# Kernel tuning notes

Hardware: AMD Instinct MI355X
Metric: run time of the kernel (lower is better)

Reference implementation:

```python
import jax, jax.numpy as jnp
import numpy as np

N, E, IN, ED, HID, HEADS, OUT, G = 50000, 800000, 128, 16, 32, 4, 64, 64
NEG_SLOPE = 0.2


def gat_conv(x, src, dst, edge_attr, W, att_src, att_dst, We, att_edge, bias,
             heads, out_ch, concat):
    """PyG-style GATConv with edge attributes and mean-filled self loops.
    src/dst already include self loops; edge_attr already includes fill rows."""
    n = x.shape[0]
    h = (x @ W).reshape(n, heads, out_ch)                      # [N,H,C]
    a_src = jnp.einsum('nhc,hc->nh', h, att_src)               # [N,H]
    a_dst = jnp.einsum('nhc,hc->nh', h, att_dst)
    eh = (edge_attr @ We).reshape(-1, heads, out_ch)           # [E',H,C]
    a_edge = jnp.einsum('ehc,hc->eh', eh, att_edge)            # [E',H]
    alpha = jax.nn.leaky_relu(a_src[src] + a_dst[dst] + a_edge, NEG_SLOPE)
    # segment softmax over incoming edges of each target node
    amax = jax.ops.segment_max(alpha, dst, num_segments=n)
    ex = jnp.exp(alpha - amax[dst])
    denom = jax.ops.segment_sum(ex, dst, num_segments=n)
    coef = ex / (denom[dst] + 1e-16)                           # [E',H]
    msg = h[src] * coef[:, :, None]                            # [E',H,C]
    out = jax.ops.segment_sum(msg, dst, num_segments=n)        # [N,H,C]
    out = out.reshape(n, heads * out_ch) if concat else out.mean(axis=1)
    return out + bias


def add_self_loops(edge_index, edge_attr, n):
    loop = jnp.arange(n, dtype=edge_index.dtype)
    src = jnp.concatenate([edge_index[0], loop])
    dst = jnp.concatenate([edge_index[1], loop])
    fill = jnp.broadcast_to(edge_attr.mean(axis=0), (n, edge_attr.shape[1]))
    ea = jnp.concatenate([edge_attr, fill], axis=0)
    return src, dst, ea


def setup_inputs() -> dict:
    key = jax.random.key(0)
    ks = jax.random.split(key, 16)
    s1 = 1.0 / np.sqrt(IN)
    s2 = 1.0 / np.sqrt(HID * HEADS)
    se = 1.0 / np.sqrt(ED)
    return {
        'x': jax.random.normal(ks[0], (N, IN), jnp.float32),
        'edge_index': jax.random.randint(ks[1], (2, E), 0, N, jnp.int64),
        'edge_attr': jax.random.normal(ks[2], (E, ED), jnp.float32),
        'batch': jnp.sort(jax.random.randint(ks[3], (N,), 0, G, jnp.int64)),
        # layer 1 params (heads=4, concat=True)
        'W1': jax.random.normal(ks[4], (IN, HEADS * HID), jnp.float32) * s1,
        'att_src1': jax.random.normal(ks[5], (HEADS, HID), jnp.float32) * s1,
        'att_dst1': jax.random.normal(ks[6], (HEADS, HID), jnp.float32) * s1,
        'We1': jax.random.normal(ks[7], (ED, HEADS * HID), jnp.float32) * se,
        'att_edge1': jax.random.normal(ks[8], (HEADS, HID), jnp.float32) * se,
        'b1': jnp.zeros((HEADS * HID,), jnp.float32),
        # layer 2 params (heads=1, concat=False)
        'W2': jax.random.normal(ks[9], (HEADS * HID, OUT), jnp.float32) * s2,
        'att_src2': jax.random.normal(ks[10], (1, OUT), jnp.float32) * s2,
        'att_dst2': jax.random.normal(ks[11], (1, OUT), jnp.float32) * s2,
        'We2': jax.random.normal(ks[12], (ED, OUT), jnp.float32) * se,
        'att_edge2': jax.random.normal(ks[13], (1, OUT), jnp.float32) * se,
        'b2': jnp.zeros((OUT,), jnp.float32),
    }


def reference(x, edge_index, edge_attr, batch,
              W1, att_src1, att_dst1, We1, att_edge1, b1,
              W2, att_src2, att_dst2, We2, att_edge2, b2):
    src, dst, ea = add_self_loops(edge_index, edge_attr, x.shape[0])
    h = gat_conv(x, src, dst, ea, W1, att_src1, att_dst1, We1, att_edge1, b1,
                 HEADS, HID, concat=True)
    h = jax.nn.elu(h)
    h = gat_conv(h, src, dst, ea, W2, att_src2, att_dst2, We2, att_edge2, b2,
                 1, OUT, concat=False)
    # global mean pool over graphs
    sums = jax.ops.segment_sum(h, batch, num_segments=G)
    cnts = jax.ops.segment_sum(jnp.ones((h.shape[0],), h.dtype), batch, num_segments=G)
    return sums / jnp.maximum(cnts, 1.0)[:, None]
```

## Files before the change

### kernel.cpp

```cpp
#include <hip/hip_runtime.h>
#include <hip/hip_fp16.h>
#include <math.h>

#define NN 50000
#define NE 800000
#define EDF 16
#define C1 128
#define HID 32
#define OUTF 64
#define NG 64
#define SLOPE 0.2f
#define NB 196
#define MAXE 256
#define PB 256
#define PCH 196
#define SEB 512
#define HB 3125

static inline int cdiv(long a, long b){ return (int)((a + b - 1) / b); }

__device__ __forceinline__ float lrelu(float x){ return x >= 0.f ? x : SLOPE * x; }

__global__ __launch_bounds__(256) void k_pre(const float* __restrict__ ea,
                                             float* __restrict__ part,
                                             const int* __restrict__ dst,
                                             int* __restrict__ deg,
                                             int* __restrict__ rank){
  int b = blockIdx.x;
  int t = threadIdx.x;
  if (b < SEB){
    const float4* ea4 = (const float4*)ea;
    const long total = (long)NE * 4;
    const long stride = (long)SEB * 256;
    float4 acc = make_float4(0.f, 0.f, 0.f, 0.f);
    for (long i = (long)b * 256 + t; i < total; i += stride * 4){
      float4 a0 = make_float4(0,0,0,0), a1 = a0, a2 = a0, a3 = a0;
      long i1 = i + stride, i2 = i + 2*stride, i3 = i + 3*stride;
      a0 = ea4[i];
      if (i1 < total) a1 = ea4[i1];
      if (i2 < total) a2 = ea4[i2];
      if (i3 < total) a3 = ea4[i3];
      acc.x += a0.x + a1.x + a2.x + a3.x;
      acc.y += a0.y + a1.y + a2.y + a3.y;
      acc.z += a0.z + a1.z + a2.z + a3.z;
      acc.w += a0.w + a1.w + a2.w + a3.w;
    }
    __shared__ float4 sp[256];
    sp[t] = acc;
    __syncthreads();
    for (int st = 128; st >= 4; st >>= 1){
      if (t < st){
        sp[t].x += sp[t+st].x; sp[t].y += sp[t+st].y;
        sp[t].z += sp[t+st].z; sp[t].w += sp[t+st].w;
      }
      __syncthreads();
    }
    if (t < 4) *(float4*)&part[b * 16 + t * 4] = sp[t];
  } else {
    long e = (long)(b - SEB) * 256 + t;
    if (e < NE) rank[e] = atomicAdd(&deg[dst[e]], 1);
  }
}

__global__ void k_scan1(const int* __restrict__ deg, int* __restrict__ rowStart,
                        int* __restrict__ blockSums,
                        const float* __restrict__ We1, const float* __restrict__ att_e1,
                        const float* __restrict__ We2, const float* __restrict__ att_e2,
                        const float* __restrict__ part,
                        float* __restrict__ M1, float* __restrict__ M2,
                        float* __restrict__ aeSL1, float* __restrict__ aeSL2){
  int t = threadIdx.x;
  if (blockIdx.x == NB){
    __shared__ float sMean[16];
    __shared__ float sM1p[64];
    if (t < 64){
      int h = t >> 4, d = t & 15;
      float s = 0.f;
      for (int c = 0; c < HID; c++) s += We1[d * C1 + h * HID + c] * att_e1[h * HID + c];
      M1[h * 16 + d] = s; sM1p[t] = s;
    }
    __shared__ float sM2p[16];
    if (t >= 64 && t < 80){
      int d = t - 64;
      float s = 0.f;
      for (int c = 0; c < OUTF; c++) s += We2[d * OUTF + c] * att_e2[c];
      M2[d] = s; sM2p[d] = s;
    }
    if (t >= 80 && t < 96){
      int c = t - 80;
      float s = 0.f;
      for (int b = 0; b < SEB; b++) s += part[b * 16 + c];
      sMean[c] = s * (1.0f / NE);
    }
    __syncthreads();
    if (t < 4){
      float s = 0.f;
      for (int d = 0; d < 16; d++) s += sMean[d] * sM1p[t * 16 + d];
      aeSL1[t] = s;
    }
    if (t == 4){
      float s = 0.f;
      for (int d = 0; d < 16; d++) s += sMean[d] * sM2p[d];
      *aeSL2 = s;
    }
    return;
  }
  __shared__ int sd[256];
  int i = blockIdx.x * 256 + t;
  int v = (i < NN) ? deg[i] : 0;
  sd[t] = v;
  __syncthreads();
  for (int off = 1; off < 256; off <<= 1){
    int add = (t >= off) ? sd[t - off] : 0;
    __syncthreads();
    sd[t] += add;
    __syncthreads();
  }
  int incl = sd[t];
  if (i < NN) rowStart[i] = incl - v;
  if (t == 255) blockSums[blockIdx.x] = incl;
}

__global__ void k_scan3(int* __restrict__ rowStart, const int* __restrict__ blockSums){
  __shared__ int sp[256];
  int t = threadIdx.x;
  int bid = blockIdx.x;
  sp[t] = (t < bid) ? blockSums[t] : 0;
  __syncthreads();
  for (int st = 128; st >= 1; st >>= 1){
    if (t < st) sp[t] += sp[t + st];
    __syncthreads();
  }
  int prefix = sp[0];
  int i = bid * 256 + t;
  if (i < NN) rowStart[i] += prefix;
  if (i == 0) rowStart[NN] = NE;
}

__global__ __launch_bounds__(256) void k_scatter(const int* __restrict__ src,
                          const int* __restrict__ dst,
                          const float* __restrict__ ea,
                          const int* __restrict__ rowStart,
                          const int* __restrict__ rank,
                          const float* __restrict__ M1, const float* __restrict__ M2,
                          unsigned int* __restrict__ recC){
  __shared__ float sM1[64];
  __shared__ float sM2[16];
  int t = threadIdx.x;
  if (t < 64) sM1[t] = M1[t];
  if (t < 16) sM2[t] = M2[t];
  __syncthreads();
  long e = (long)blockIdx.x * 256 + t;
  if (e >= NE) return;
  int d = dst[e];
  int s = src[e];
  int rk = rank[e];
  float eav[16];
  const float4* p = (const float4*)(ea + e * EDF);
  *(float4*)&eav[0]  = p[0]; *(float4*)&eav[4]  = p[1];
  *(float4*)&eav[8]  = p[2]; *(float4*)&eav[12] = p[3];
  int pos = rowStart[d] + rk;
  float ae[4];
#pragma unroll
  for (int h = 0; h < 4; h++){
    float sdot = 0.f;
#pragma unroll
    for (int dd = 0; dd < 16; dd++) sdot += eav[dd] * sM1[h * 16 + dd];
    ae[h] = sdot;
  }
  float a2 = 0.f;
#pragma unroll
  for (int dd = 0; dd < 16; dd++) a2 += eav[dd] * sM2[dd];
  __half2 ae01 = __floats2half2_rn(ae[0], ae[1]);
  __half2 ae23 = __floats2half2_rn(ae[2], ae[3]);
  __half  a2h  = __float2half_rn(a2);
  uint4 rec;
  rec.x = (unsigned)s | ((unsigned)*(unsigned short*)&a2h << 16);
  rec.y = *(unsigned*)&ae01;
  rec.z = *(unsigned*)&ae23;
  rec.w = 0u;
  *(uint4*)&recC[(long)pos * 4] = rec;
}

__global__ __launch_bounds__(256) void k_gemm1(const float* __restrict__ A,
                                               const float* __restrict__ B,
                                               __half* __restrict__ Ch,
                                               const float* __restrict__ attS,
                                               const float* __restrict__ attD,
                                               float* __restrict__ aS, float* __restrict__ aD){
  __shared__ float As[16][64];
  __shared__ float Bs[16][64];
  const int M = NN, Ncols = C1, K = 128;
  int tid = threadIdx.x;
  int row0 = blockIdx.x * 64, col0 = blockIdx.y * 64;
  int tx = tid & 15, ty = tid >> 4;
  int lrow = tid >> 2, lkq = tid & 3;
  int bk = tid >> 4, bc = tid & 15;
  float acc[4][4] = {};
  for (int k0 = 0; k0 < K; k0 += 16){
    float4 a4 = make_float4(0.f, 0.f, 0.f, 0.f);
    int gr = row0 + lrow;
    if (gr < M) a4 = *(const float4*)&A[(long)gr * K + k0 + lkq * 4];
    As[lkq * 4 + 0][lrow] = a4.x; As[lkq * 4 + 1][lrow] = a4.y;
    As[lkq * 4 + 2][lrow] = a4.z; As[lkq * 4 + 3][lrow] = a4.w;
    *(float4*)&Bs[bk][bc * 4] = *(const float4*)&B[(long)(k0 + bk) * Ncols + col0 + bc * 4];
    __syncthreads();
#pragma unroll
    for (int k = 0; k < 16; k++){
      float4 a = *(float4*)&As[k][ty * 4];
      float4 b = *(float4*)&Bs[k][tx * 4];
      acc[0][0] += a.x*b.x; acc[0][1] += a.x*b.y; acc[0][2] += a.x*b.z; acc[0][3] += a.x*b.w;
      acc[1][0] += a.y*b.x; acc[1][1] += a.y*b.y; acc[1][2] += a.y*b.z; acc[1][3] += a.y*b.w;
      acc[2][0] += a.z*b.x; acc[2][1] += a.z*b.y; acc[2][2] += a.z*b.z; acc[2][3] += a.z*b.w;
      acc[3][0] += a.w*b.x; acc[3][1] += a.w*b.y; acc[3][2] += a.w*b.z; acc[3][3] += a.w*b.w;
    }
    __syncthreads();
  }
#pragma unroll
  for (int i = 0; i < 4; i++){
    int r = row0 + ty * 4 + i;
    if (r < M){
      __half2 p0 = __floats2half2_rn(acc[i][0], acc[i][1]);
      __half2 p1 = __floats2half2_rn(acc[i][2], acc[i][3]);
      uint2 pk; pk.x = *(unsigned*)&p0; pk.y = *(unsigned*)&p1;
      *(uint2*)&Ch[(long)r * Ncols + col0 + tx * 4] = pk;
    }
  }
  float4 avS = *(const float4*)&attS[col0 + tx * 4];
  float4 avD = *(const float4*)&attD[col0 + tx * 4];
  float ss[4], sd[4];
#pragma unroll
  for (int i = 0; i < 4; i++){
    ss[i] = acc[i][0]*avS.x + acc[i][1]*avS.y + acc[i][2]*avS.z + acc[i][3]*avS.w;
    sd[i] = acc[i][0]*avD.x + acc[i][1]*avD.y + acc[i][2]*avD.z + acc[i][3]*avD.w;
  }
#pragma unroll
  for (int off = 1; off <= 4; off <<= 1){
#pragma unroll
    for (int i = 0; i < 4; i++){
      ss[i] += __shfl_xor(ss[i], off);
      sd[i] += __shfl_xor(sd[i], off);
    }
  }
  if ((tx & 7) == 0){
    int head = blockIdx.y * 2 + (tx >> 3);
#pragma unroll
    for (int i = 0; i < 4; i++){
      int r = row0 + ty * 4 + i;
      if (r < M){ aS[(long)r * 4 + head] = ss[i]; aD[(long)r * 4 + head] = sd[i]; }
    }
  }
}

__global__ __launch_bounds__(256) void k_gemm2(const __half* __restrict__ Ah,
                                               const float* __restrict__ B,
                                               __half* __restrict__ Ch,
                                               const float* __restrict__ attS,
                                               const float* __restrict__ attD,
                                               float* __restrict__ aS, float* __restrict__ aD){
  __shared__ float As[16][64];
  __shared__ float Bs[16][64];
  const int M = NN, Ncols = OUTF, K = 128;
  int tid = threadIdx.x;
  int row0 = blockIdx.x * 64, col0 = 0;
  int tx = tid & 15, ty = tid >> 4;
  int lrow = tid >> 2, lkq = tid & 3;
  int bk = tid >> 4, bc = tid & 15;
  float acc[4][4] = {};
  for (int k0 = 0; k0 < K; k0 += 16){
    float4 a4 = make_float4(0.f, 0.f, 0.f, 0.f);
    int gr = row0 + lrow;
    if (gr < M){
      uint2 u = *(const uint2*)&Ah[(long)gr * K + k0 + lkq * 4];
      float2 f0 = __half22float2(*(__half2*)&u.x);
      float2 f1 = __half22float2(*(__half2*)&u.y);
      a4 = make_float4(f0.x, f0.y, f1.x, f1.y);
    }
    As[lkq * 4 + 0][lrow] = a4.x; As[lkq * 4 + 1][lrow] = a4.y;
    As[lkq * 4 + 2][lrow] = a4.z; As[lkq * 4 + 3][lrow] = a4.w;
    *(float4*)&Bs[bk][bc * 4] = *(const float4*)&B[(long)(k0 + bk) * Ncols + col0 + bc * 4];
    __syncthreads();
#pragma unroll
    for (int k = 0; k < 16; k++){
      float4 a = *(float4*)&As[k][ty * 4];
      float4 b = *(float4*)&Bs[k][tx * 4];
      acc[0][0] += a.x*b.x; acc[0][1] += a.x*b.y; acc[0][2] += a.x*b.z; acc[0][3] += a.x*b.w;
      acc[1][0] += a.y*b.x; acc[1][1] += a.y*b.y; acc[1][2] += a.y*b.z; acc[1][3] += a.y*b.w;
      acc[2][0] += a.z*b.x; acc[2][1] += a.z*b.y; acc[2][2] += a.z*b.z; acc[2][3] += a.z*b.w;
      acc[3][0] += a.w*b.x; acc[3][1] += a.w*b.y; acc[3][2] += a.w*b.z; acc[3][3] += a.w*b.w;
    }
    __syncthreads();
  }
#pragma unroll
  for (int i = 0; i < 4; i++){
    int r = row0 + ty * 4 + i;
    if (r < M){
      __half2 p0 = __floats2half2_rn(acc[i][0], acc[i][1]);
      __half2 p1 = __floats2half2_rn(acc[i][2], acc[i][3]);
      uint2 pk; pk.x = *(unsigned*)&p0; pk.y = *(unsigned*)&p1;
      *(uint2*)&Ch[(long)r * Ncols + tx * 4] = pk;
    }
  }
  float4 avS = *(const float4*)&attS[tx * 4];
  float4 avD = *(const float4*)&attD[tx * 4];
  float ss[4], sd[4];
#pragma unroll
  for (int i = 0; i < 4; i++){
    ss[i] = acc[i][0]*avS.x + acc[i][1]*avS.y + acc[i][2]*avS.z + acc[i][3]*avS.w;
    sd[i] = acc[i][0]*avD.x + acc[i][1]*avD.y + acc[i][2]*avD.z + acc[i][3]*avD.w;
  }
#pragma unroll
  for (int off = 1; off <= 8; off <<= 1){
#pragma unroll
    for (int i = 0; i < 4; i++){
      ss[i] += __shfl_xor(ss[i], off);
      sd[i] += __shfl_xor(sd[i], off);
    }
  }
  if (tx == 0){
#pragma unroll
    for (int i = 0; i < 4; i++){
      int r = row0 + ty * 4 + i;
      if (r < M){ aS[r] = ss[i]; aD[r] = sd[i]; }
    }
  }
}

__global__ __launch_bounds__(256) void k_agg1(
    const int* __restrict__ rowStart, const unsigned int* __restrict__ recC,
    const float* __restrict__ a_src, const float* __restrict__ a_dst,
    const float* __restrict__ aeSL1,
    const __half* __restrict__ h1h, const float* __restrict__ b1,
    __half* __restrict__ out1h){
  __shared__ int   sS[4][MAXE];
  __shared__ float sC[4][MAXE * 4];
  int wid = threadIdx.x >> 6;
  int lane = threadIdx.x & 63;
  int n = blockIdx.x * 4 + wid;
  int start = rowStart[n];
  int dg = rowStart[n + 1] - start;
  float4 sl4 = *(const float4*)aeSL1;
  float4 ad4 = *(const float4*)(a_dst + (long)n * 4);
  float4 as4 = *(const float4*)(a_src + (long)n * 4);
  float4 cSelf;
  cSelf.x = __expf(lrelu(as4.x + ad4.x + sl4.x));
  cSelf.y = __expf(lrelu(as4.y + ad4.y + sl4.y));
  cSelf.z = __expf(lrelu(as4.z + ad4.z + sl4.z));
  cSelf.w = __expf(lrelu(as4.w + ad4.w + sl4.w));
  float4 dsum = make_float4(0.f, 0.f, 0.f, 0.f);
  for (int j0 = 0; j0 < dg; j0 += 64){
    int j = j0 + lane;
    if (j < dg){
      uint4 rec = *(const uint4*)&recC[(long)(start + j) * 4];
      int s = rec.x & 0xffff;
      float2 ae01 = __half22float2(*(__half2*)&rec.y);
      float2 ae23 = __half22float2(*(__half2*)&rec.z);
      float4 asv = *(const float4*)(a_src + (long)s * 4);
      float4 c;
      c.x = __expf(lrelu(asv.x + ad4.x + ae01.x));
      c.y = __expf(lrelu(asv.y + ad4.y + ae01.y));
      c.z = __expf(lrelu(asv.z + ad4.z + ae23.x));
      c.w = __expf(lrelu(asv.w + ad4.w + ae23.y));
      dsum.x += c.x; dsum.y += c.y; dsum.z += c.z; dsum.w += c.w;
      if (j < MAXE){
        sS[wid][j] = s << 6;
        *(float4*)&sC[wid][j * 4] = c;
      }
    }
  }
#pragma unroll
  for (int off = 32; off > 0; off >>= 1){
    dsum.x += __shfl_xor(dsum.x, off);
    dsum.y += __shfl_xor(dsum.y, off);
    dsum.z += __shfl_xor(dsum.z, off);
    dsum.w += __shfl_xor(dsum.w, off);
  }
  float adA[4] = {ad4.x, ad4.y, ad4.z, ad4.w};
  float csA[4] = {cSelf.x, cSelf.y, cSelf.z, cSelf.w};
  float invA[4];
  invA[0] = 1.f / (dsum.x + cSelf.x + 1e-16f);
  invA[1] = 1.f / (dsum.y + cSelf.y + 1e-16f);
  invA[2] = 1.f / (dsum.z + cSelf.z + 1e-16f);
  invA[3] = 1.f / (dsum.w + cSelf.w + 1e-16f);
  int ch = lane * 2;
  int h = lane >> 4;
  const unsigned int* hrow = (const unsigned int*)h1h;
  float cs   = csA[h];
  float vinv = invA[h];
  float adh  = adA[h];
  unsigned int hv = hrow[(unsigned)(n * 64 + lane)];
  float2 hf = __half22float2(*(__half2*)&hv);
  float acc0 = hf.x * cs, acc1 = hf.y * cs;
  int jmax = dg < MAXE ? dg : MAXE;
  int j = 0;
  for (; j + 4 <= jmax; j += 4){
    int o0 = sS[wid][j+0], o1 = sS[wid][j+1], o2 = sS[wid][j+2], o3 = sS[wid][j+3];
    float c0 = sC[wid][(j+0)*4+h], c1 = sC[wid][(j+1)*4+h];
    float c2 = sC[wid][(j+2)*4+h], c3 = sC[wid][(j+3)*4+h];
    unsigned int v0 = hrow[(unsigned)(o0 + lane)];
    unsigned int v1 = hrow[(unsigned)(o1 + lane)];
    unsigned int v2 = hrow[(unsigned)(o2 + lane)];
    unsigned int v3 = hrow[(unsigned)(o3 + lane)];
    float2 f0 = __half22float2(*(__half2*)&v0);
    float2 f1 = __half22float2(*(__half2*)&v1);
    float2 f2 = __half22float2(*(__half2*)&v2);
    float2 f3 = __half22float2(*(__half2*)&v3);
    acc0 += c0 * f0.x + c1 * f1.x + c2 * f2.x + c3 * f3.x;
    acc1 += c0 * f0.y + c1 * f1.y + c2 * f2.y + c3 * f3.y;
  }
  for (; j < jmax; j++){
    int o = sS[wid][j];
    float c = sC[wid][j * 4 + h];
    unsigned int v = hrow[(unsigned)(o + lane)];
    float2 f = __half22float2(*(__half2*)&v);
    acc0 += c * f.x; acc1 += c * f.y;
  }
  for (; j < dg; j++){
    uint4 rec = *(const uint4*)&recC[(long)(start + j) * 4];
    int s = rec.x & 0xffff;
    float2 ae01 = __half22float2(*(__half2*)&rec.y);
    float2 ae23 = __half22float2(*(__half2*)&rec.z);
    float aeA[4] = {ae01.x, ae01.y, ae23.x, ae23.y};
    float asv = a_src[(long)s * 4 + h];
    float c = __expf(lrelu(asv + adh + aeA[h]));
    unsigned int v = hrow[(unsigned)((s << 6) + lane)];
    float2 f = __half22float2(*(__half2*)&v);
    acc0 += c * f.x; acc1 += c * f.y;
  }
  float v0 = acc0 * vinv + b1[ch];
  float v1 = acc1 * vinv + b1[ch + 1];
  v0 = v0 > 0.f ? v0 : __expf(v0) - 1.f;
  v1 = v1 > 0.f ? v1 : __expf(v1) - 1.f;
  __half2 pk = __floats2half2_rn(v0, v1);
  ((unsigned int*)out1h)[(unsigned)(n * 64 + lane)] = *(unsigned*)&pk;
}

__global__ __launch_bounds__(256) void k_agg2(
    const int* __restrict__ rowStart, const unsigned int* __restrict__ recC,
    const float* __restrict__ a_src, const float* __restrict__ a_dst,
    const float* __restrict__ aeSL2,
    const __half* __restrict__ h2h, float* __restrict__ out2){
  __shared__ int   sS[4][MAXE];
  __shared__ float sC[4][MAXE];
  int wid = threadIdx.x >> 6;
  int lane = threadIdx.x & 63;
  int n = blockIdx.x * 4 + wid;
  int start = rowStart[n];
  int dg = rowStart[n + 1] - start;
  float adN = a_dst[n];
  float cSelf = __expf(lrelu(a_src[n] + adN + *aeSL2));
  float dsum = 0.f;
  for (int j0 = 0; j0 < dg; j0 += 64){
    int j = j0 + lane;
    if (j < dg){
      unsigned rx = recC[(long)(start + j) * 4];
      int s = rx & 0xffff;
      unsigned short ah = (unsigned short)(rx >> 16);
      float c = __expf(lrelu(a_src[s] + adN + __half2float(*(__half*)&ah)));
      dsum += c;
      if (j < MAXE){ sS[wid][j] = s << 6; sC[wid][j] = c; }
    }
  }
#pragma unroll
  for (int off = 32; off > 0; off >>= 1) dsum += __shfl_xor(dsum, off);
  float inv = 1.f / (dsum + cSelf + 1e-16f);
  float acc = __half2float(h2h[(unsigned)(n * 64 + lane)]) * cSelf;
  int jmax = dg < MAXE ? dg : MAXE;
  int j = 0;
  for (; j + 4 <= jmax; j += 4){
    int o0 = sS[wid][j+0], o1 = sS[wid][j+1], o2 = sS[wid][j+2], o3 = sS[wid][j+3];
    float c0 = sC[wid][j+0], c1 = sC[wid][j+1], c2 = sC[wid][j+2], c3 = sC[wid][j+3];
    float f0 = __half2float(h2h[(unsigned)(o0 + lane)]);
    float f1 = __half2float(h2h[(unsigned)(o1 + lane)]);
    float f2 = __half2float(h2h[(unsigned)(o2 + lane)]);
    float f3 = __half2float(h2h[(unsigned)(o3 + lane)]);
    acc += c0 * f0 + c1 * f1 + c2 * f2 + c3 * f3;
  }
  for (; j < jmax; j++)
    acc += sC[wid][j] * __half2float(h2h[(unsigned)(sS[wid][j] + lane)]);
  for (; j < dg; j++){
    unsigned rx = recC[(long)(start + j) * 4];
    int s = rx & 0xffff;
    unsigned short ah = (unsigned short)(rx >> 16);
    float c = __expf(lrelu(a_src[s] + adN + __half2float(*(__half*)&ah)));
    acc += c * __half2float(h2h[(unsigned)((s << 6) + lane)]);
  }
  out2[(long)n * OUTF + lane] = acc * inv;
}

__global__ __launch_bounds__(256) void k_pool1(const float* __restrict__ out2,
                                               const int* __restrict__ batch,
                                               float* __restrict__ gsum){
  int c = threadIdx.x & 63, r = threadIdx.x >> 6;
  int n0 = blockIdx.x * PCH + r;
  int n1 = blockIdx.x * PCH + PCH; if (n1 > NN) n1 = NN;
  float acc = 0.f; int curG = -1;
  for (int n = n0; n < n1; n += 4){
    int g = batch[n];
    if (g != curG){
      if (curG >= 0) atomicAdd(&gsum[curG * 64 + c], acc);
      curG = g; acc = 0.f;
    }
    acc += out2[(long)n * OUTF + c];
  }
  if (curG >= 0) atomicAdd(&gsum[curG * 64 + c], acc);
}

__global__ void k_pool2(const float* __restrict__ gsum, const int* __restrict__ batch,
                        const float* __restrict__ b2, float* __restrict__ out){
  int g = blockIdx.x;
  int c = threadIdx.x;
  int lo = 0, hi = NN;
  while (lo < hi){ int mid = (lo + hi) >> 1; if (batch[mid] < g) lo = mid + 1; else hi = mid; }
  int a = lo, b = NN;
  while (a < b){ int mid = (a + b) >> 1; if (batch[mid] < g + 1) a = mid + 1; else b = mid; }
  int cnt = a - lo;
  out[g * 64 + c] = (gsum[g * 64 + c] + (float)cnt * b2[c]) / fmaxf((float)cnt, 1.0f);
}

extern "C" void kernel_launch(void* const* d_in, const int* in_sizes, int n_in,
                              void* d_out, int out_size, void* d_ws, size_t ws_size,
                              hipStream_t stream) {
  const float* x         = (const float*)d_in[0];
  const int*   eidx      = (const int*)d_in[1];
  const float* edge_attr = (const float*)d_in[2];
  const int*   batch     = (const int*)d_in[3];
  const float* W1        = (const float*)d_in[4];
  const float* att_src1  = (const float*)d_in[5];
  const float* att_dst1  = (const float*)d_in[6];
  const float* We1       = (const float*)d_in[7];
  const float* att_edge1 = (const float*)d_in[8];
  const float* b1        = (const float*)d_in[9];
  const float* W2        = (const float*)d_in[10];
  const float* att_src2  = (const float*)d_in[11];
  const float* att_dst2  = (const float*)d_in[12];
  const float* We2       = (const float*)d_in[13];
  const float* att_edge2 = (const float*)d_in[14];
  const float* b2        = (const float*)d_in[15];
  const int* srcI = eidx;
  const int* dstI = eidx + NE;

  float* ws = (float*)d_ws;
  __half* h1h   = (__half*)ws;
  __half* out1h = (__half*)(ws + 3200000);
  float* out2   = ws + 6400000;
  float* a_src1 = ws + 9600000;
  float* a_dst1 = a_src1 + (long)NN * 4;
  unsigned int* recC = (unsigned int*)(a_dst1 + (long)NN * 4);
  int*   deg    = (int*)(recC + (long)NE * 4);
  float* gsum   = (float*)(deg + NN);
  int*   rowStart = (int*)(gsum + NG * 64);
  int*   blockSums = rowStart + 50004;
  float* part   = (float*)(blockSums + 260);
  float* M1     = part + SEB * 16;
  float* M2v    = M1 + 64;
  float* aeSL1  = M2v + 16;
  float* aeSL2  = aeSL1 + 4;
  int*   rank   = (int*)(aeSL2 + 4);
  __half* h2h = h1h;
  float* a_src2 = a_src1; float* a_dst2 = a_dst1;

  hipMemsetAsync(deg, 0, (NN + NG * 64) * sizeof(int), stream);
  k_pre<<<SEB + HB, 256, 0, stream>>>(edge_attr, part, dstI, deg, rank);
  k_scan1<<<NB + 1, 256, 0, stream>>>(deg, rowStart, blockSums,
                                      We1, att_edge1, We2, att_edge2, part,
                                      M1, M2v, aeSL1, aeSL2);
  k_scan3<<<NB, 256, 0, stream>>>(rowStart, blockSums);
  k_scatter<<<cdiv(NE, 256), 256, 0, stream>>>(srcI, dstI, edge_attr, rowStart, rank,
                                               M1, M2v, recC);
  k_gemm1<<<dim3(cdiv(NN, 64), 2), 256, 0, stream>>>(x, W1, h1h, att_src1, att_dst1,
                                                     a_src1, a_dst1);
  k_agg1<<<NN / 4, 256, 0, stream>>>(rowStart, recC, a_src1, a_dst1, aeSL1,
                                     h1h, b1, out1h);
  k_gemm2<<<dim3(cdiv(NN, 64), 1), 256, 0, stream>>>(out1h, W2, h2h, att_src2, att_dst2,
                                                     a_src2, a_dst2);
  k_agg2<<<NN / 4, 256, 0, stream>>>(rowStart, recC, a_src2, a_dst2, aeSL2,
                                     h2h, out2);
  k_pool1<<<PB, 256, 0, stream>>>(out2, batch, gsum);
  k_pool2<<<NG, 64, 0, stream>>>(gsum, batch, b2, (float*)d_out);
}
```

Baseline: 342.3 us.

## Fuse layer-1 GEMM into preprocessing kernel and pad degree counters

Merges the layer-1 feature GEMM into the edge-attribute reduction and degree-counting kernel as extra blocks, so the independent GEMM runs concurrently with the atomic-heavy degree pass and one launch is dropped. Degree counters are spread 16 ints apart to cut atomic contention and false sharing on the same cache lines. Shared A tiles are padded to 68 columns to reduce LDS bank conflicts. The cost is a 16x larger degree array to memset and scan with strided reads, and more register pressure in the combined kernel.

```diff
diff --git a/kernel.cpp b/kernel.cpp
--- a/kernel.cpp
+++ b/kernel.cpp
@@ -16,16 +16,19 @@
 #define PCH 196
 #define SEB 512
 #define HB 3125
+#define GB1 1564
 
 static inline int cdiv(long a, long b){ return (int)((a + b - 1) / b); }
 
 __device__ __forceinline__ float lrelu(float x){ return x >= 0.f ? x : SLOPE * x; }
 
-__global__ __launch_bounds__(256) void k_pre(const float* __restrict__ ea,
-                                             float* __restrict__ part,
-                                             const int* __restrict__ dst,
-                                             int* __restrict__ deg,
-                                             int* __restrict__ rank){
+__global__ __launch_bounds__(256) void k_pg(
+    const float* __restrict__ ea, float* __restrict__ part,
+    const int* __restrict__ dst, int* __restrict__ degP, int* __restrict__ rank,
+    const float* __restrict__ A, const float* __restrict__ B,
+    __half* __restrict__ Ch, const float* __restrict__ attS,
+    const float* __restrict__ attD,
+    float* __restrict__ aS, float* __restrict__ aD){
   int b = blockIdx.x;
   int t = threadIdx.x;
   if (b < SEB){
@@ -56,13 +59,78 @@
       __syncthreads();
     }
     if (t < 4) *(float4*)&part[b * 16 + t * 4] = sp[t];
-  } else {
+    return;
+  }
+  if (b < SEB + HB){
     long e = (long)(b - SEB) * 256 + t;
-    if (e < NE) rank[e] = atomicAdd(&deg[dst[e]], 1);
-  }
-}
-
-__global__ void k_scan1(const int* __restrict__ deg, int* __restrict__ rowStart,
+    if (e < NE) rank[e] = atomicAdd(&degP[dst[e] << 4], 1);
+    return;
+  }
+  __shared__ float As[16][68];
+  __shared__ float Bs[16][64];
+  const int M = NN, Ncols = C1, K = 128;
+  int bg = b - (SEB + HB);
+  int row0 = (bg >> 1) * 64, col0 = (bg & 1) * 64;
+  int tx = t & 15, ty = t >> 4;
+  int lrow = t >> 2, lkq = t & 3;
+  int bk = t >> 4, bc = t & 15;
+  float acc[4][4] = {};
+  for (int k0 = 0; k0 < K; k0 += 16){
+    float4 a4 = make_float4(0.f, 0.f, 0.f, 0.f);
+    int gr = row0 + lrow;
+    if (gr < M) a4 = *(const float4*)&A[(long)gr * K + k0 + lkq * 4];
+    As[lkq * 4 + 0][lrow] = a4.x; As[lkq * 4 + 1][lrow] = a4.y;
+    As[lkq * 4 + 2][lrow] = a4.z; As[lkq * 4 + 3][lrow] = a4.w;
+    *(float4*)&Bs[bk][bc * 4] = *(const float4*)&B[(long)(k0 + bk) * Ncols + col0 + bc * 4];
+    __syncthreads();
+#pragma unroll
+    for (int k = 0; k < 16; k++){
+      float4 a = *(float4*)&As[k][ty * 4];
+      float4 bb = *(float4*)&Bs[k][tx * 4];
+      acc[0][0] += a.x*bb.x; acc[0][1] += a.x*bb.y; acc[0][2] += a.x*bb.z; acc[0][3] += a.x*bb.w;
+      acc[1][0] += a.y*bb.x; acc[1][1] += a.y*bb.y; acc[1][2] += a.y*bb.z; acc[1][3] += a.y*bb.w;
+      acc[2][0] += a.z*bb.x; acc[2][1] += a.z*bb.y; acc[2][2] += a.z*bb.z; acc[2][3] += a.z*bb.w;
+      acc[3][0] += a.w*bb.x; acc[3][1] += a.w*bb.y; acc[3][2] += a.w*bb.z; acc[3][3] += a.w*bb.w;
+    }
+    __syncthreads();
+  }
+#pragma unroll
+  for (int i = 0; i < 4; i++){
+    int r = row0 + ty * 4 + i;
+    if (r < M){
+      __half2 p0 = __floats2half2_rn(acc[i][0], acc[i][1]);
+      __half2 p1 = __floats2half2_rn(acc[i][2], acc[i][3]);
+      uint2 pk; pk.x = *(unsigned*)&p0; pk.y = *(unsigned*)&p1;
+      *(uint2*)&Ch[(long)r * Ncols + col0 + tx * 4] = pk;
+    }
+  }
+  float4 avS = *(const float4*)&attS[col0 + tx * 4];
+  float4 avD = *(const float4*)&attD[col0 + tx * 4];
+  float ss[4], sd[4];
+#pragma unroll
+  for (int i = 0; i < 4; i++){
+    ss[i] = acc[i][0]*avS.x + acc[i][1]*avS.y + acc[i][2]*avS.z + acc[i][3]*avS.w;
+    sd[i] = acc[i][0]*avD.x + acc[i][1]*avD.y + acc[i][2]*avD.z + acc[i][3]*avD.w;
+  }
+#pragma unroll
+  for (int off = 1; off <= 4; off <<= 1){
+#pragma unroll
+    for (int i = 0; i < 4; i++){
+      ss[i] += __shfl_xor(ss[i], off);
+      sd[i] += __shfl_xor(sd[i], off);
+    }
+  }
+  if ((tx & 7) == 0){
+    int head = (bg & 1) * 2 + (tx >> 3);
+#pragma unroll
+    for (int i = 0; i < 4; i++){
+      int r = row0 + ty * 4 + i;
+      if (r < M){ aS[(long)r * 4 + head] = ss[i]; aD[(long)r * 4 + head] = sd[i]; }
+    }
+  }
+}
+
+__global__ void k_scan1(const int* __restrict__ degP, int* __restrict__ rowStart,
                         int* __restrict__ blockSums,
                         const float* __restrict__ We1, const float* __restrict__ att_e1,
                         const float* __restrict__ We2, const float* __restrict__ att_e2,
@@ -107,7 +175,7 @@
   }
   __shared__ int sd[256];
   int i = blockIdx.x * 256 + t;
-  int v = (i < NN) ? deg[i] : 0;
+  int v = (i < NN) ? degP[i << 4] : 0;
   sd[t] = v;
   __syncthreads();
   for (int off = 1; off < 256; off <<= 1){
@@ -182,83 +250,13 @@
   *(uint4*)&recC[(long)pos * 4] = rec;
 }
 
-__global__ __launch_bounds__(256) void k_gemm1(const float* __restrict__ A,
-                                               const float* __restrict__ B,
-                                               __half* __restrict__ Ch,
-                                               const float* __restrict__ attS,
-                                               const float* __restrict__ attD,
-                                               float* __restrict__ aS, float* __restrict__ aD){
-  __shared__ float As[16][64];
-  __shared__ float Bs[16][64];
-  const int M = NN, Ncols = C1, K = 128;
-  int tid = threadIdx.x;
-  int row0 = blockIdx.x * 64, col0 = blockIdx.y * 64;
-  int tx = tid & 15, ty = tid >> 4;
-  int lrow = tid >> 2, lkq = tid & 3;
-  int bk = tid >> 4, bc = tid & 15;
-  float acc[4][4] = {};
-  for (int k0 = 0; k0 < K; k0 += 16){
-    float4 a4 = make_float4(0.f, 0.f, 0.f, 0.f);
-    int gr = row0 + lrow;
-    if (gr < M) a4 = *(const float4*)&A[(long)gr * K + k0 + lkq * 4];
-    As[lkq * 4 + 0][lrow] = a4.x; As[lkq * 4 + 1][lrow] = a4.y;
-    As[lkq * 4 + 2][lrow] = a4.z; As[lkq * 4 + 3][lrow] = a4.w;
-    *(float4*)&Bs[bk][bc * 4] = *(const float4*)&B[(long)(k0 + bk) * Ncols + col0 + bc * 4];
-    __syncthreads();
-#pragma unroll
-    for (int k = 0; k < 16; k++){
-      float4 a = *(float4*)&As[k][ty * 4];
-      float4 b = *(float4*)&Bs[k][tx * 4];
-      acc[0][0] += a.x*b.x; acc[0][1] += a.x*b.y; acc[0][2] += a.x*b.z; acc[0][3] += a.x*b.w;
-      acc[1][0] += a.y*b.x; acc[1][1] += a.y*b.y; acc[1][2] += a.y*b.z; acc[1][3] += a.y*b.w;
-      acc[2][0] += a.z*b.x; acc[2][1] += a.z*b.y; acc[2][2] += a.z*b.z; acc[2][3] += a.z*b.w;
-      acc[3][0] += a.w*b.x; acc[3][1] += a.w*b.y; acc[3][2] += a.w*b.z; acc[3][3] += a.w*b.w;
-    }
-    __syncthreads();
-  }
-#pragma unroll
-  for (int i = 0; i < 4; i++){
-    int r = row0 + ty * 4 + i;
-    if (r < M){
-      __half2 p0 = __floats2half2_rn(acc[i][0], acc[i][1]);
-      __half2 p1 = __floats2half2_rn(acc[i][2], acc[i][3]);
-      uint2 pk; pk.x = *(unsigned*)&p0; pk.y = *(unsigned*)&p1;
-      *(uint2*)&Ch[(long)r * Ncols + col0 + tx * 4] = pk;
-    }
-  }
-  float4 avS = *(const float4*)&attS[col0 + tx * 4];
-  float4 avD = *(const float4*)&attD[col0 + tx * 4];
-  float ss[4], sd[4];
-#pragma unroll
-  for (int i = 0; i < 4; i++){
-    ss[i] = acc[i][0]*avS.x + acc[i][1]*avS.y + acc[i][2]*avS.z + acc[i][3]*avS.w;
-    sd[i] = acc[i][0]*avD.x + acc[i][1]*avD.y + acc[i][2]*avD.z + acc[i][3]*avD.w;
-  }
-#pragma unroll
-  for (int off = 1; off <= 4; off <<= 1){
-#pragma unroll
-    for (int i = 0; i < 4; i++){
-      ss[i] += __shfl_xor(ss[i], off);
-      sd[i] += __shfl_xor(sd[i], off);
-    }
-  }
-  if ((tx & 7) == 0){
-    int head = blockIdx.y * 2 + (tx >> 3);
-#pragma unroll
-    for (int i = 0; i < 4; i++){
-      int r = row0 + ty * 4 + i;
-      if (r < M){ aS[(long)r * 4 + head] = ss[i]; aD[(long)r * 4 + head] = sd[i]; }
-    }
-  }
-}
-
 __global__ __launch_bounds__(256) void k_gemm2(const __half* __restrict__ Ah,
                                                const float* __restrict__ B,
                                                __half* __restrict__ Ch,
                                                const float* __restrict__ attS,
                                                const float* __restrict__ attD,
                                                float* __restrict__ aS, float* __restrict__ aD){
-  __shared__ float As[16][64];
+  __shared__ float As[16][68];
   __shared__ float Bs[16][64];
   const int M = NN, Ncols = OUTF, K = 128;
   int tid = threadIdx.x;
@@ -283,11 +281,11 @@
 #pragma unroll
     for (int k = 0; k < 16; k++){
       float4 a = *(float4*)&As[k][ty * 4];
-      float4 b = *(float4*)&Bs[k][tx * 4];
-      acc[0][0] += a.x*b.x; acc[0][1] += a.x*b.y; acc[0][2] += a.x*b.z; acc[0][3] += a.x*b.w;
-      acc[1][0] += a.y*b.x; acc[1][1] += a.y*b.y; acc[1][2] += a.y*b.z; acc[1][3] += a.y*b.w;
-      acc[2][0] += a.z*b.x; acc[2][1] += a.z*b.y; acc[2][2] += a.z*b.z; acc[2][3] += a.z*b.w;
-      acc[3][0] += a.w*b.x; acc[3][1] += a.w*b.y; acc[3][2] += a.w*b.z; acc[3][3] += a.w*b.w;
+      float4 bb = *(float4*)&Bs[k][tx * 4];
+      acc[0][0] += a.x*bb.x; acc[0][1] += a.x*bb.y; acc[0][2] += a.x*bb.z; acc[0][3] += a.x*bb.w;
+      acc[1][0] += a.y*bb.x; acc[1][1] += a.y*bb.y; acc[1][2] += a.y*bb.z; acc[1][3] += a.y*bb.w;
+      acc[2][0] += a.z*bb.x; acc[2][1] += a.z*bb.y; acc[2][2] += a.z*bb.z; acc[2][3] += a.z*bb.w;
+      acc[3][0] += a.w*bb.x; acc[3][1] += a.w*bb.y; acc[3][2] += a.w*bb.z; acc[3][3] += a.w*bb.w;
     }
     __syncthreads();
   }
@@ -547,8 +545,8 @@
   float* a_src1 = ws + 9600000;
   float* a_dst1 = a_src1 + (long)NN * 4;
   unsigned int* recC = (unsigned int*)(a_dst1 + (long)NN * 4);
-  int*   deg    = (int*)(recC + (long)NE * 4);
-  float* gsum   = (float*)(deg + NN);
+  int*   degP   = (int*)(recC + (long)NE * 4);
+  float* gsum   = (float*)(degP + (long)NN * 16);
   int*   rowStart = (int*)(gsum + NG * 64);
   int*   blockSums = rowStart + 50004;
   float* part   = (float*)(blockSums + 260);
@@ -560,20 +558,20 @@
   __half* h2h = h1h;
   float* a_src2 = a_src1; float* a_dst2 = a_dst1;
 
-  hipMemsetAsync(deg, 0, (NN + NG * 64) * sizeof(int), stream);
-  k_pre<<<SEB + HB, 256, 0, stream>>>(edge_attr, part, dstI, deg, rank);
-  k_scan1<<<NB + 1, 256, 0, stream>>>(deg, rowStart, blockSums,
+  hipMemsetAsync(degP, 0, ((long)NN * 16 + NG * 64) * sizeof(int), stream);
+  k_pg<<<SEB + HB + GB1, 256, 0, stream>>>(edge_attr, part, dstI, degP, rank,
+                                           x, W1, h1h, att_src1, att_dst1,
+                                           a_src1, a_dst1);
+  k_scan1<<<NB + 1, 256, 0, stream>>>(degP, rowStart, blockSums,
                                       We1, att_edge1, We2, att_edge2, part,
                                       M1, M2v, aeSL1, aeSL2);
   k_scan3<<<NB, 256, 0, stream>>>(rowStart, blockSums);
-  k_scatter<<<cdiv(NE, 256), 256, 0, stream>>>(srcI, dstI, edge_attr, rowStart, rank,
-                                               M1, M2v, recC);
-  k_gemm1<<<dim3(cdiv(NN, 64), 2), 256, 0, stream>>>(x, W1, h1h, att_src1, att_dst1,
-                                                     a_src1, a_dst1);
+  k_scatter<<<HB, 256, 0, stream>>>(srcI, dstI, edge_attr, rowStart, rank,
+                                    M1, M2v, recC);
   k_agg1<<<NN / 4, 256, 0, stream>>>(rowStart, recC, a_src1, a_dst1, aeSL1,
                                      h1h, b1, out1h);
-  k_gemm2<<<dim3(cdiv(NN, 64), 1), 256, 0, stream>>>(out1h, W2, h2h, att_src2, att_dst2,
-                                                     a_src2, a_dst2);
+  k_gemm2<<<cdiv(NN, 64), 256, 0, stream>>>(out1h, W2, h2h, att_src2, att_dst2,
+                                            a_src2, a_dst2);
   k_agg2<<<NN / 4, 256, 0, stream>>>(rowStart, recC, a_src2, a_dst2, aeSL2,
                                      h2h, out2);
   k_pool1<<<PB, 256, 0, stream>>>(out2, batch, gsum);
```

Result: no change. 339.9 us (-0.7%).
